# Optimization experiments

Hardware: AMD Instinct MI355X
Metric: run time of the kernel (lower is better)

## Reference

```python
import jax, jax.numpy as jnp
import numpy as np

WIDTH = 1024
NH = 16
HD = 64
MBS = 16
B = 4
L = 2048
BASE_LR = 1.0
EPS = 1e-6


def gelu_tanh(x):
    return jax.nn.gelu(x, approximate=True)


def gelu_bwd(x):
    t = jnp.tanh(0.79788456 * x * (1 + 0.044715 * x * x))
    return 0.5 * x * ((1 - t * t) * (0.79788456 + 0.1070322243 * x * x)) + 0.5 * (1 + t)


def ln_fwd(x, g, b):
    mu = x.mean(-1, keepdims=True)
    var = ((x - mu) ** 2).mean(-1, keepdims=True)
    return g * ((x - mu) * jax.lax.rsqrt(var + EPS)) + b


def ln_l2_bwd(x, tgt, g, b):
    # grad of 0.5*||LN(x)-tgt||^2 wrt x
    mu = x.mean(-1, keepdims=True)
    var = ((x - mu) ** 2).mean(-1, keepdims=True)
    std = jnp.sqrt(var + EPS)
    xh = (x - mu) / std
    gx = (g * xh + b - tgt) * g
    return (gx - gx.mean(-1, keepdims=True) - xh * (gx * xh).mean(-1, keepdims=True)) / std


def adapter_forward(hidden_states, Wq, Wk, Wv, Wo, Wg, lr_w, lr_b,
                    learnable_token_idx, norm_w, norm_b, W1, b1, W2, b2,
                    post_w, post_b):
    Bb, Ll, width = hidden_states.shape
    nh, hd = norm_w.shape
    mbs = learnable_token_idx.shape[0]
    nc = Ll // mbs  # L chosen divisible by mini_batch_size

    def split_heads(x):  # [B,L,width] -> [B,nh,nc,mbs,hd]
        return x.reshape(Bb, Ll, nh, hd).transpose(0, 2, 1, 3).reshape(Bb, nh, nc, mbs, hd)

    XQ = split_heads(hidden_states @ Wq.T)
    XK = split_heads(hidden_states @ Wk.T)
    XV = split_heads(hidden_states @ Wv.T)

    # eta: learnable per-token lr gate (get_eta)
    X = hidden_states.reshape(Bb, nc, mbs, width)
    lr = jnp.einsum('bnkc,hdc->bhnkd', X, lr_w) + lr_b.reshape(1, nh, 1, 1, 1)
    lr = jax.nn.sigmoid(lr).transpose(0, 1, 2, 4, 3)  # [B,nh,nc,1,mbs]
    lr_eta = BASE_LR * lr / hd
    token_idx = jnp.clip(1.0 / jnp.arange(1, mbs + 1, dtype=hidden_states.dtype)
                         + learnable_token_idx, 0.0, None)
    token_eta = token_idx.reshape(1, 1, 1, mbs, 1)
    eta = token_eta * lr_eta  # [B,nh,nc,mbs,mbs]

    tril = jnp.tril(jnp.ones((mbs, mbs), dtype=hidden_states.dtype))
    lnw = norm_w.reshape(nh, 1, hd)
    lnb = norm_b.reshape(nh, 1, hd)

    def step(carry, xs):
        W1s, b1s, W2s, b2s = carry  # [B,nh,hd,4hd], [B,nh,1,4hd], [B,nh,4hd,hd], [B,nh,1,hd]
        XQm, XKm, XVm, etam = xs    # [B,nh,mbs,hd] x3, [B,nh,mbs,mbs]
        X1 = XKm
        Z1 = X1 @ W1s + b1s
        X2 = gelu_tanh(Z1)
        Z2 = X2 @ W2s + b2s
        gZ2 = ln_l2_bwd(Z2, XVm - XKm, lnw, lnb)
        gZ1 = (gZ2 @ jnp.swapaxes(W2s, -1, -2)) * gelu_bwd(Z1)
        eta_tril = etam * tril
        Attn1 = tril * (XQm @ jnp.swapaxes(X1, -1, -2))
        b1_bar = b1s - eta_tril @ gZ1
        Z1_bar = XQm @ W1s - (etam * Attn1) @ gZ1 + b1_bar
        X2_bar = gelu_tanh(Z1_bar)
        Attn2 = tril * (X2_bar @ jnp.swapaxes(X2, -1, -2))
        b2_bar = b2s - eta_tril @ gZ2
        Z2_bar = X2_bar @ W2s - (etam * Attn2) @ gZ2 + b2_bar
        last = etam[:, :, -1, :, None]  # [B,nh,mbs,1]
        W1n = W1s - jnp.swapaxes(last * X1, -1, -2) @ gZ1
        b1n = b1s - (last * gZ1).sum(-2, keepdims=True)
        W2n = W2s - jnp.swapaxes(last * X2, -1, -2) @ gZ2
        b2n = b2s - (last * gZ2).sum(-2, keepdims=True)
        XQW = XQm + ln_fwd(Z2_bar, lnw, lnb)
        return (W1n, b1n, W2n, b2n), XQW

    carry0 = (jnp.broadcast_to(W1, (Bb,) + W1.shape),
              jnp.broadcast_to(b1, (Bb,) + b1.shape),
              jnp.broadcast_to(W2, (Bb,) + W2.shape),
              jnp.broadcast_to(b2, (Bb,) + b2.shape))
    xs = tuple(jnp.moveaxis(t, 2, 0) for t in (XQ, XK, XV, eta))
    _, XQW = jax.lax.scan(step, carry0, xs)  # [nc,B,nh,mbs,hd]
    out = XQW.transpose(1, 0, 3, 2, 4).reshape(Bb, Ll, width)

    # post_norm (LayerNorm eps=1e-6)
    out = ln_fwd(out, post_w, post_b)
    # gate
    out = gelu_tanh(hidden_states @ Wg.T) * out
    # o_proj
    return out @ Wo.T


def setup_inputs():
    key = jax.random.key(0)
    ks = jax.random.split(key, 10)
    n = lambda k, s: jax.random.normal(k, s, dtype=jnp.float32) * 0.02
    return {
        'hidden_states': jax.random.normal(ks[0], (B, L, WIDTH), dtype=jnp.float32),
        'Wq': n(ks[1], (WIDTH, WIDTH)),
        'Wk': n(ks[2], (WIDTH, WIDTH)),
        'Wv': n(ks[3], (WIDTH, WIDTH)),
        'Wo': n(ks[4], (WIDTH, WIDTH)),
        'Wg': n(ks[5], (WIDTH, WIDTH)),
        'lr_w': n(ks[6], (NH, 1, WIDTH)),
        'lr_b': jnp.zeros((NH, 1), jnp.float32),
        'learnable_token_idx': jnp.zeros((MBS,), jnp.float32),
        'norm_w': jnp.ones((NH, HD), jnp.float32),
        'norm_b': jnp.zeros((NH, HD), jnp.float32),
        'W1': n(ks[7], (NH, HD, 4 * HD)),
        'b1': jnp.zeros((NH, 1, 4 * HD), jnp.float32),
        'W2': n(ks[8], (NH, 4 * HD, HD)),
        'b2': jnp.zeros((NH, 1, HD), jnp.float32),
        'post_w': jnp.ones((WIDTH,), jnp.float32),
        'post_b': jnp.zeros((WIDTH,), jnp.float32),
    }


def reference(hidden_states, Wq, Wk, Wv, Wo, Wg, lr_w, lr_b, learnable_token_idx,
              norm_w, norm_b, W1, b1, W2, b2, post_w, post_b):
    return adapter_forward(hidden_states, Wq, Wk, Wv, Wo, Wg, lr_w, lr_b,
                           learnable_token_idx, norm_w, norm_b, W1, b1, W2, b2,
                           post_w, post_b)
```

## Files before the change

kernel.cpp:

```cpp
#include <hip/hip_runtime.h>

#define WIDTH 1024
#define MBSZ 16
#define LLL 2048
#define NCHUNK 128

typedef __attribute__((ext_vector_type(4))) float f32x4;
typedef __attribute__((ext_vector_type(2))) float f32x2;
typedef __attribute__((ext_vector_type(8))) short short8;
typedef __attribute__((ext_vector_type(4))) short short4v;
typedef __attribute__((ext_vector_type(2))) unsigned u32x2;
typedef __attribute__((ext_vector_type(4))) unsigned u32x4;

#define MFMA16(a, b, c) __builtin_amdgcn_mfma_f32_16x16x32_bf16((a), (b), (c), 0, 0, 0)

__device__ __forceinline__ short f2bf(float f) {
  unsigned u = __float_as_uint(f);
  u = (u + 0x7FFFu + ((u >> 16) & 1u)) >> 16;
  return (short)u;
}
__device__ __forceinline__ float bf2f(short s) {
  return __uint_as_float(((unsigned)(unsigned short)s) << 16);
}
__device__ __forceinline__ unsigned cvt_pk(float lo, float hi) {
  unsigned r;
  asm("v_cvt_pk_bf16_f32 %0, %1, %2" : "=v"(r) : "v"(lo), "v"(hi));
  return r;
}
__device__ __forceinline__ float fast_e2u(float x) {
  return __builtin_amdgcn_exp2f(x * (2.30220776f + 0.10294322f * x * x));
}
__device__ __forceinline__ float gelu_f(float x) {
  float e = fast_e2u(x);
  return x * (1.0f - __builtin_amdgcn_rcpf(e + 1.0f));
}
__device__ __forceinline__ float gelu_bwd_f(float x) {
  float e = fast_e2u(x);
  float r = __builtin_amdgcn_rcpf(e + 1.0f);
  return 2.0f * x * r * (1.0f - r) * (0.79788456f + 0.1070322243f * x * x) + (1.0f - r);
}
__device__ __forceinline__ int w2row(int d) { return d * 264 + (d >> 3) * 24; }

__global__ __launch_bounds__(256) void cvt_kernel(const float* __restrict__ hs,
                                                  const float* __restrict__ Wq,
                                                  const float* __restrict__ Wk,
                                                  const float* __restrict__ Wv,
                                                  const float* __restrict__ Wg,
                                                  const float* __restrict__ Wo,
                                                  short* __restrict__ dst) {
  const long idx = ((long)blockIdx.x * 256 + threadIdx.x) * 8;
  if (idx >= 13631488L) return;
  const float* src;
  long off;
  if (idx < 8388608L)       { src = hs; off = idx; }
  else if (idx < 9437184L)  { src = Wq; off = idx - 8388608L; }
  else if (idx < 10485760L) { src = Wk; off = idx - 9437184L; }
  else if (idx < 11534336L) { src = Wv; off = idx - 10485760L; }
  else if (idx < 12582912L) { src = Wg; off = idx - 11534336L; }
  else                      { src = Wo; off = idx - 12582912L; }
  const f32x4 a = *(const f32x4*)(src + off);
  const f32x4 b = *(const f32x4*)(src + off + 4);
  u32x4 o;
  o[0] = cvt_pk(a[0], a[1]); o[1] = cvt_pk(a[2], a[3]);
  o[2] = cvt_pk(b[0], b[1]); o[3] = cvt_pk(b[2], b[3]);
  *(u32x4*)(dst + idx) = o;
}

template <int OUTBF>
__global__ __launch_bounds__(256) void gemm_bt_b(const short* __restrict__ A,
                                                 const short* __restrict__ W,
                                                 float* __restrict__ C,
                                                 short* __restrict__ Cb) {
  __shared__ __align__(16) short sA[64][40];
  __shared__ __align__(16) short sB[64][40];
  const int tid = threadIdx.x;
  const int m0 = blockIdx.x * 64, n0 = blockIdx.y * 64;
  const int srow = tid >> 2, sk = (tid & 3) * 8;
  const int wv = tid >> 6, ln = tid & 63;
  const int fr = ln & 15, kh = (ln >> 4) * 8;
  f32x4 acc[4];
#pragma unroll
  for (int s = 0; s < 4; ++s) acc[s] = (f32x4){0.f, 0.f, 0.f, 0.f};
  const short* ga = A + (long)(m0 + srow) * 1024 + sk;
  const short* gw = W + (long)(n0 + srow) * 1024 + sk;
  for (int k0 = 0; k0 < 1024; k0 += 32) {
    const short8 a8 = *(const short8*)(ga + k0);
    const short8 w8 = *(const short8*)(gw + k0);
    *(short8*)&sA[srow][sk] = a8;
    *(short8*)&sB[srow][sk] = w8;
    __syncthreads();
    short8 af = *(const short8*)&sA[wv * 16 + fr][kh];
#pragma unroll
    for (int s = 0; s < 4; ++s) {
      short8 bf8 = *(const short8*)&sB[s * 16 + fr][kh];
      acc[s] = MFMA16(af, bf8, acc[s]);
    }
    __syncthreads();
  }
  const int orow = m0 + wv * 16 + (ln >> 4) * 4;
#pragma unroll
  for (int s = 0; s < 4; ++s)
#pragma unroll
    for (int q = 0; q < 4; ++q) {
      if (OUTBF)
        Cb[(long)(orow + q) * 1024 + n0 + s * 16 + fr] = f2bf(acc[s][q]);
      else
        C[(long)(orow + q) * 1024 + n0 + s * 16 + fr] = acc[s][q];
    }
}

__global__ __launch_bounds__(256) void lr_kernel(const float* __restrict__ hs,
                                                 const float* __restrict__ lrw,
                                                 const float* __restrict__ lrb,
                                                 float* __restrict__ out) {
  __shared__ __align__(16) float row[1024];
  const int t = blockIdx.x, tid = threadIdx.x;
  *(f32x4*)&row[tid * 4] = *(const f32x4*)&hs[(long)t * 1024 + tid * 4];
  __syncthreads();
  const int hh = tid >> 4, j = tid & 15;
  const float* wrow = lrw + hh * 1024;
  float s = 0.f;
#pragma unroll 4
  for (int m = 0; m < 16; ++m) {
    const int c = j * 4 + m * 64;
    f32x4 x = *(const f32x4*)&row[c];
    f32x4 w = *(const f32x4*)&wrow[c];
    s += x[0] * w[0] + x[1] * w[1] + x[2] * w[2] + x[3] * w[3];
  }
#pragma unroll
  for (int o = 8; o; o >>= 1) s += __shfl_xor(s, o, 16);
  if (j == 0) {
    const float v = s + lrb[hh];
    const float sg = 1.f / (1.f + expf(-v));
    const int b = t >> 11, tr = t & 2047;
    out[((b << 4) + hh) * 2048 + tr] = sg * (1.f / 64.f);
  }
}

__global__ __launch_bounds__(512, 2) void scan_kernel(
    float* __restrict__ Qb, const float* __restrict__ Kb, const float* __restrict__ Vb,
    const float* __restrict__ LRb, const float* __restrict__ lti,
    const float* __restrict__ nw, const float* __restrict__ nb,
    const float* __restrict__ W1in, const float* __restrict__ b1in,
    const float* __restrict__ W2in, const float* __restrict__ b2in) {
  __shared__ __align__(16) short sW1b[256 * 72];
  __shared__ __align__(16) short sW2dp[64 * 264 + 192];
  __shared__ __align__(16) short la1T[64 * 24];
  __shared__ __align__(16) short la2T[256 * 24];
  __shared__ __align__(16) short sX1b[16 * 72];
  __shared__ __align__(16) short sXQb[16 * 72];
  __shared__ __align__(16) float sXQf[16 * 68];
  __shared__ __align__(16) float sTg[16 * 72];
  __shared__ __align__(16) short sX2b[16 * 264];
  __shared__ __align__(16) short sXbb[16 * 264];
  __shared__ __align__(16) short sG1c[256 * 24];
  __shared__ __align__(16) short sG2b[16 * 72];
  __shared__ __align__(16) short sG2c[64 * 24];
  __shared__ __align__(16) float sZ2f[16 * 68];
  __shared__ __align__(16) short sC1b[16 * 24];
  __shared__ __align__(16) short sC2b[16 * 24];
  __shared__ __align__(16) float sB1[256];
  __shared__ __align__(16) float sB2[64];
  __shared__ float sLr[16];
  __shared__ float sTok[16];
  __shared__ __align__(16) float sLnw[64];
  __shared__ __align__(16) float sLnb[64];

  const int bh = blockIdx.x, b = bh >> 4, h = bh & 15;
  const int tid = threadIdx.x;
  const int w = tid >> 6, ln = tid & 63;
  const int fr = ln & 15, half = ln >> 4, hk = half * 8;
  const int nt0 = 2 * w;

  float w1m[8][4], w2m[8][4];
#pragma unroll
  for (int r = 0; r < 8; ++r) {
    const int T = w * 8 + r, dt = T >> 4, pt = T & 15;
#pragma unroll
    for (int qq = 0; qq < 4; ++qq) {
      w1m[r][qq] = W1in[h * 16384 + (dt * 16 + half * 4 + qq) * 256 + pt * 16 + fr];
      w2m[r][qq] = W2in[h * 16384 + (pt * 16 + half * 4 + qq) * 64 + dt * 16 + fr];
    }
  }
  for (int e = tid; e < 16384; e += 512) {
    {
      const int d = e >> 8, p = e & 255;
      sW1b[p * 72 + d] = f2bf(W1in[h * 16384 + e]);
    }
    {
      const int p = e >> 6, d = e & 63;
      sW2dp[w2row(d) + (p ^ (((d >> 3) & 3) << 3))] = f2bf(W2in[h * 16384 + e]);
    }
  }
  if (tid < 256) sB1[tid] = b1in[h * 256 + tid];
  if (tid < 64) { sB2[tid] = b2in[h * 64 + tid]; sLnw[tid] = nw[h * 64 + tid]; sLnb[tid] = nb[h * 64 + tid]; }
  if (tid < 16) sTok[tid] = fmaxf(1.0f / (float)(tid + 1) + lti[tid], 0.0f);

  const f32x4 zf4 = (f32x4){0.f, 0.f, 0.f, 0.f};
  short8 zs8;
#pragma unroll
  for (int j = 0; j < 8; ++j) zs8[j] = 0;

  const int pf_i = tid >> 5;
  const int pf_d = (tid & 31) * 2;
  f32x2 pk, pq, pv;
  float plr = 0.f;
  {
    const long a0 = ((long)(b * LLL + pf_i)) * WIDTH + h * 64 + pf_d;
    pk = *(const f32x2*)&Kb[a0];
    pq = *(const f32x2*)&Qb[a0];
    pv = *(const f32x2*)&Vb[a0];
    if (tid < 16) plr = LRb[(long)bh * 2048 + tid];
  }

  for (int n = 0; n < NCHUNK; ++n) {
    const long gbase = ((long)(b * LLL + n * MBSZ)) * WIDTH + h * 64;

    {
      *(unsigned*)&sX1b[pf_i * 72 + pf_d] = cvt_pk(pk[0], pk[1]);
      *(unsigned*)&sXQb[pf_i * 72 + pf_d] = cvt_pk(pq[0], pq[1]);
      sXQf[pf_i * 68 + pf_d] = pq[0];
      sXQf[pf_i * 68 + pf_d + 1] = pq[1];
      sTg[pf_i * 72 + pf_d] = pv[0] - pk[0];
      sTg[pf_i * 72 + pf_d + 1] = pv[1] - pk[1];
      if (tid < 16) sLr[tid] = plr;
    }
    __syncthreads();

    short8 aX1[2], aXQ[2];
    aX1[0] = *(const short8*)&sX1b[fr * 72 + hk];
    aX1[1] = *(const short8*)&sX1b[fr * 72 + 32 + hk];
    aXQ[0] = *(const short8*)&sXQb[fr * 72 + hk];
    aXQ[1] = *(const short8*)&sXQb[fr * 72 + 32 + hk];
    f32x4 z1[2], q1[2];
    float b1p[2];
#pragma unroll
    for (int t = 0; t < 2; ++t) {
      const int p = (nt0 + t) * 16 + fr;
      z1[t] = zf4; q1[t] = zf4;
#pragma unroll
      for (int ks = 0; ks < 2; ++ks) {
        short8 bw = *(const short8*)&sW1b[p * 72 + ks * 32 + hk];
        z1[t] = MFMA16(aX1[ks], bw, z1[t]);
        q1[t] = MFMA16(aXQ[ks], bw, q1[t]);
      }
      b1p[t] = sB1[p];
#pragma unroll
      for (int qq = 0; qq < 4; ++qq) {
        z1[t][qq] += b1p[t];
        sX2b[(half * 4 + qq) * 264 + p] = f2bf(gelu_f(z1[t][qq]));
      }
    }
    {
      const float tok15 = sTok[15];
      const int d = tid >> 3, j0 = (tid & 7) * 2;
      const float v0 = bf2f(sX1b[j0 * 72 + d]) * (tok15 * sLr[j0]);
      const float v1 = bf2f(sX1b[(j0 + 1) * 72 + d]) * (tok15 * sLr[j0 + 1]);
      *(unsigned*)&la1T[d * 24 + j0] = cvt_pk(v0, v1);
    }
    if (w == 0) {
      f32x4 c = MFMA16(aXQ[0], aX1[0], zf4);
      c = MFMA16(aXQ[1], aX1[1], c);
#pragma unroll
      for (int qq = 0; qq < 4; ++qq) {
        const int i = half * 4 + qq, j = fr;
        sC1b[i * 24 + j] = f2bf((i >= j) ? sTok[i] * sLr[j] * (c[qq] + 1.0f) : 0.0f);
      }
    }
    __syncthreads();

    float bb2old = 0.f;
    if (w < 4) {
      const int d = w * 16 + fr;
      const int sw = ((d >> 3) & 3) << 3;
      const int rb = w2row(d);
      f32x4 za = zf4, zb = zf4;
#pragma unroll
      for (int ks = 0; ks < 4; ++ks) {
        short8 a = *(const short8*)&sX2b[fr * 264 + ks * 32 + hk];
        short8 bfr = *(const short8*)&sW2dp[rb + ((ks * 32 + hk) ^ sw)];
        za = MFMA16(a, bfr, za);
      }
#pragma unroll
      for (int ks = 4; ks < 8; ++ks) {
        short8 a = *(const short8*)&sX2b[fr * 264 + ks * 32 + hk];
        short8 bfr = *(const short8*)&sW2dp[rb + ((ks * 32 + hk) ^ sw)];
        zb = MFMA16(a, bfr, zb);
      }
      bb2old = sB2[d];
#pragma unroll
      for (int qq = 0; qq < 4; ++qq)
        sZ2f[(half * 4 + qq) * 68 + d] = za[qq] + zb[qq] + bb2old;
    }
    __syncthreads();

    if (tid < 256) {
      const int i = tid >> 4, j4 = tid & 15;
      const f32x4 z = *(const f32x4*)&sZ2f[i * 68 + j4 * 4];
      float s1 = z[0] + z[1] + z[2] + z[3];
      float s2 = z[0] * z[0] + z[1] * z[1] + z[2] * z[2] + z[3] * z[3];
#pragma unroll
      for (int o = 8; o; o >>= 1) { s1 += __shfl_xor(s1, o, 16); s2 += __shfl_xor(s2, o, 16); }
      const float mu = s1 * (1.f / 64.f);
      const float rstd = rsqrtf(s2 * (1.f / 64.f) - mu * mu + 1e-6f);
      const f32x4 g = *(const f32x4*)&sLnw[j4 * 4];
      const f32x4 bb = *(const f32x4*)&sLnb[j4 * 4];
      const f32x4 tg = *(const f32x4*)&sTg[i * 72 + j4 * 4];
      f32x4 xh, gx;
      float a1 = 0.f, a2 = 0.f;
#pragma unroll
      for (int e = 0; e < 4; ++e) {
        xh[e] = (z[e] - mu) * rstd;
        gx[e] = (g[e] * xh[e] + bb[e] - tg[e]) * g[e];
        a1 += gx[e]; a2 += gx[e] * xh[e];
      }
#pragma unroll
      for (int o = 8; o; o >>= 1) { a1 += __shfl_xor(a1, o, 16); a2 += __shfl_xor(a2, o, 16); }
      const float m1 = a1 * (1.f / 64.f), m2 = a2 * (1.f / 64.f);
      float o4[4];
#pragma unroll
      for (int e = 0; e < 4; ++e) o4[e] = (gx[e] - m1 - xh[e] * m2) * rstd;
      const unsigned lo = cvt_pk(o4[0], o4[1]);
      const unsigned hi = cvt_pk(o4[2], o4[3]);
      *(u32x2*)&sG2b[i * 72 + j4 * 4] = (u32x2){lo, hi};
      sG2c[(j4 * 4 + 0) * 24 + i] = (short)lo;
      sG2c[(j4 * 4 + 1) * 24 + i] = (short)(lo >> 16);
      sG2c[(j4 * 4 + 2) * 24 + i] = (short)hi;
      sG2c[(j4 * 4 + 3) * 24 + i] = (short)(hi >> 16);
    } else {
      const int pp = tid - 256;
      const float tok15 = sTok[15];
      unsigned uu[8];
#pragma unroll
      for (int jp = 0; jp < 8; ++jp) {
        const float v0 = bf2f(sX2b[(2 * jp) * 264 + pp]) * (tok15 * sLr[2 * jp]);
        const float v1 = bf2f(sX2b[(2 * jp + 1) * 264 + pp]) * (tok15 * sLr[2 * jp + 1]);
        uu[jp] = cvt_pk(v0, v1);
      }
      *(u32x4*)&la2T[pp * 24] = (u32x4){uu[0], uu[1], uu[2], uu[3]};
      *(u32x4*)&la2T[pp * 24 + 8] = (u32x4){uu[4], uu[5], uu[6], uu[7]};
    }
    __syncthreads();

    {
      short8 aG2[2];
      aG2[0] = *(const short8*)&sG2b[fr * 72 + hk];
      aG2[1] = *(const short8*)&sG2b[fr * 72 + 32 + hk];
#pragma unroll
      for (int t = 0; t < 2; ++t) {
        const int p = (nt0 + t) * 16 + fr;
        f32x4 g = zf4;
#pragma unroll
        for (int ks = 0; ks < 2; ++ks) {
          const int dg = ks * 32 + hk;
          const int rb = w2row(dg) + (p ^ (((dg >> 3) & 3) << 3));
          short8 bw;
#pragma unroll
          for (int jj = 0; jj < 8; ++jj) bw[jj] = sW2dp[rb + jj * 264];
          g = MFMA16(aG2[ks], bw, g);
        }
        const unsigned lo = cvt_pk(g[0] * gelu_bwd_f(z1[t][0]), g[1] * gelu_bwd_f(z1[t][1]));
        const unsigned hi = cvt_pk(g[2] * gelu_bwd_f(z1[t][2]), g[3] * gelu_bwd_f(z1[t][3]));
        *(u32x2*)&sG1c[p * 24 + half * 4] = (u32x2){lo, hi};
      }
    }
    if (tid < 64) {
      float s = 0.f;
#pragma unroll
      for (int j = 0; j < 16; ++j) s += sLr[j] * bf2f(sG2c[tid * 24 + j]);
      sB2[tid] -= sTok[15] * s;
    }
    __syncthreads();

    {
      short8 ac = zs8;
      if (half < 2) ac = *(const short8*)&sC1b[fr * 24 + hk];
#pragma unroll
      for (int t = 0; t < 2; ++t) {
        const int p = (nt0 + t) * 16 + fr;
        short8 bg = zs8;
        if (half < 2) bg = *(const short8*)&sG1c[p * 24 + hk];
        f32x4 corr = MFMA16(ac, bg, zf4);
#pragma unroll
        for (int qq = 0; qq < 4; ++qq)
          sXbb[(half * 4 + qq) * 264 + p] = f2bf(gelu_f(q1[t][qq] + b1p[t] - corr[qq]));
      }
    }
    {
#pragma unroll
      for (int r = 0; r < 8; ++r) {
        const int T = w * 8 + r, dt = T >> 4, pt = T & 15;
        short8 af = zs8, bg = zs8;
        if (half < 2) {
          af = *(const short8*)&la1T[(dt * 16 + fr) * 24 + hk];
          bg = *(const short8*)&sG1c[(pt * 16 + fr) * 24 + hk];
        }
        f32x4 dl = MFMA16(af, bg, zf4);
        const int pp = pt * 16 + fr, d0 = dt * 16 + half * 4;
        w1m[r][0] -= dl[0]; w1m[r][1] -= dl[1]; w1m[r][2] -= dl[2]; w1m[r][3] -= dl[3];
        const unsigned lo = cvt_pk(w1m[r][0], w1m[r][1]);
        const unsigned hi = cvt_pk(w1m[r][2], w1m[r][3]);
        *(u32x2*)&sW1b[pp * 72 + d0] = (u32x2){lo, hi};
      }
    }
    if (tid < 256) {
      float s = 0.f;
#pragma unroll
      for (int j = 0; j < 16; ++j) s += sLr[j] * bf2f(sG1c[tid * 24 + j]);
      sB1[tid] -= sTok[15] * s;
    }
    __syncthreads();

    {
      const int nn = (n + 1 < NCHUNK) ? n + 1 : n;
      const long a1 = ((long)(b * LLL + nn * MBSZ + pf_i)) * WIDTH + h * 64 + pf_d;
      pk = *(const f32x2*)&Kb[a1];
      pq = *(const f32x2*)&Qb[a1];
      pv = *(const f32x2*)&Vb[a1];
      if (tid < 16) plr = LRb[(long)bh * 2048 + nn * MBSZ + tid];
    }
    f32x4 zbar = zf4;
    if (w < 4) {
      const int d = w * 16 + fr;
      const int sw = ((d >> 3) & 3) << 3;
      const int rb = w2row(d);
      f32x4 za = zf4, zb = zf4;
#pragma unroll
      for (int ks = 0; ks < 4; ++ks) {
        short8 a = *(const short8*)&sXbb[fr * 264 + ks * 32 + hk];
        short8 bfr = *(const short8*)&sW2dp[rb + ((ks * 32 + hk) ^ sw)];
        za = MFMA16(a, bfr, za);
      }
#pragma unroll
      for (int ks = 4; ks < 8; ++ks) {
        short8 a = *(const short8*)&sXbb[fr * 264 + ks * 32 + hk];
        short8 bfr = *(const short8*)&sW2dp[rb + ((ks * 32 + hk) ^ sw)];
        zb = MFMA16(a, bfr, zb);
      }
      zbar[0] = za[0] + zb[0]; zbar[1] = za[1] + zb[1];
      zbar[2] = za[2] + zb[2]; zbar[3] = za[3] + zb[3];
    } else if (w == 4) {
      f32x4 c = zf4;
#pragma unroll
      for (int ks = 0; ks < 8; ++ks) {
        short8 a = *(const short8*)&sXbb[fr * 264 + ks * 32 + hk];
        short8 bx = *(const short8*)&sX2b[fr * 264 + ks * 32 + hk];
        c = MFMA16(a, bx, c);
      }
#pragma unroll
      for (int qq = 0; qq < 4; ++qq) {
        const int i = half * 4 + qq, j = fr;
        sC2b[i * 24 + j] = f2bf((i >= j) ? sTok[i] * sLr[j] * (c[qq] + 1.0f) : 0.0f);
      }
    }
    __syncthreads();

    if (w < 4) {
      const int d = w * 16 + fr;
      short8 ac = zs8, bg = zs8;
      if (half < 2) {
        ac = *(const short8*)&sC2b[fr * 24 + hk];
        bg = *(const short8*)&sG2c[d * 24 + hk];
      }
      f32x4 corr = MFMA16(ac, bg, zf4);
#pragma unroll
      for (int qq = 0; qq < 4; ++qq)
        sZ2f[(half * 4 + qq) * 68 + d] = zbar[qq] + bb2old - corr[qq];
    }
    {
#pragma unroll
      for (int r = 0; r < 8; ++r) {
        const int T = w * 8 + r, pt = T & 15, dt = T >> 4;
        short8 af = zs8, bg = zs8;
        if (half < 2) {
          af = *(const short8*)&la2T[(pt * 16 + fr) * 24 + hk];
          bg = *(const short8*)&sG2c[(dt * 16 + fr) * 24 + hk];
        }
        f32x4 dl = MFMA16(af, bg, zf4);
        const int dd = dt * 16 + fr;
        const int swp = ((dd >> 3) & 3) << 3;
        const int p0 = pt * 16 + half * 4;
        w2m[r][0] -= dl[0]; w2m[r][1] -= dl[1]; w2m[r][2] -= dl[2]; w2m[r][3] -= dl[3];
        const unsigned lo = cvt_pk(w2m[r][0], w2m[r][1]);
        const unsigned hi = cvt_pk(w2m[r][2], w2m[r][3]);
        *(u32x2*)&sW2dp[w2row(dd) + (p0 ^ swp)] = (u32x2){lo, hi};
      }
    }
    __syncthreads();

    if (tid < 256) {
      const int i = tid >> 4, j4 = tid & 15;
      const f32x4 z = *(const f32x4*)&sZ2f[i * 68 + j4 * 4];
      float s1 = z[0] + z[1] + z[2] + z[3];
      float s2 = z[0] * z[0] + z[1] * z[1] + z[2] * z[2] + z[3] * z[3];
#pragma unroll
      for (int o = 8; o; o >>= 1) { s1 += __shfl_xor(s1, o, 16); s2 += __shfl_xor(s2, o, 16); }
      const float mu = s1 * (1.f / 64.f);
      const float rstd = rsqrtf(s2 * (1.f / 64.f) - mu * mu + 1e-6f);
      const f32x4 g = *(const f32x4*)&sLnw[j4 * 4];
      const f32x4 bb = *(const f32x4*)&sLnb[j4 * 4];
      const f32x4 xq = *(const f32x4*)&sXQf[i * 68 + j4 * 4];
      f32x4 o4;
#pragma unroll
      for (int e = 0; e < 4; ++e) o4[e] = xq[e] + g[e] * ((z[e] - mu) * rstd) + bb[e];
      *(f32x4*)&Qb[gbase + (long)i * WIDTH + j4 * 4] = o4;
    }
    __syncthreads();
  }
}

__global__ __launch_bounds__(256) void epi_kernel(const float* __restrict__ X,
                                                  const short* __restrict__ G,
                                                  const float* __restrict__ pw,
                                                  const float* __restrict__ pb,
                                                  short* __restrict__ T) {
  __shared__ float red[8];
  const int t = blockIdx.x, tid = threadIdx.x;
  const long base = (long)t * 1024 + tid * 4;
  f32x4 x = *(const f32x4*)&X[base];
  float s1 = x[0] + x[1] + x[2] + x[3];
  float s2 = x[0] * x[0] + x[1] * x[1] + x[2] * x[2] + x[3] * x[3];
#pragma unroll
  for (int o = 32; o; o >>= 1) { s1 += __shfl_xor(s1, o, 64); s2 += __shfl_xor(s2, o, 64); }
  const int wv = tid >> 6, ln = tid & 63;
  if (ln == 0) { red[wv] = s1; red[4 + wv] = s2; }
  __syncthreads();
  s1 = red[0] + red[1] + red[2] + red[3];
  s2 = red[4] + red[5] + red[6] + red[7];
  const float mu = s1 * (1.f / 1024.f);
  const float rstd = rsqrtf(s2 * (1.f / 1024.f) - mu * mu + 1e-6f);
  const short4v g4 = *(const short4v*)&G[base];
  f32x4 w = *(const f32x4*)&pw[tid * 4];
  f32x4 bb = *(const f32x4*)&pb[tid * 4];
  float o4[4];
#pragma unroll
  for (int e = 0; e < 4; ++e) {
    float y = w[e] * ((x[e] - mu) * rstd) + bb[e];
    o4[e] = gelu_f(bf2f(g4[e])) * y;
  }
  *(u32x2*)&T[base] = (u32x2){cvt_pk(o4[0], o4[1]), cvt_pk(o4[2], o4[3])};
}

extern "C" void kernel_launch(void* const* d_in, const int* in_sizes, int n_in,
                              void* d_out, int out_size, void* d_ws, size_t ws_size,
                              hipStream_t stream) {
  const float* hs  = (const float*)d_in[0];
  const float* Wq  = (const float*)d_in[1];
  const float* Wk  = (const float*)d_in[2];
  const float* Wv  = (const float*)d_in[3];
  const float* Wo  = (const float*)d_in[4];
  const float* Wg  = (const float*)d_in[5];
  const float* lrw = (const float*)d_in[6];
  const float* lrb = (const float*)d_in[7];
  const float* lti = (const float*)d_in[8];
  const float* nw  = (const float*)d_in[9];
  const float* nb  = (const float*)d_in[10];
  const float* W1  = (const float*)d_in[11];
  const float* b1  = (const float*)d_in[12];
  const float* W2  = (const float*)d_in[13];
  const float* b2  = (const float*)d_in[14];
  const float* pw  = (const float*)d_in[15];
  const float* pb  = (const float*)d_in[16];
  float* out = (float*)d_out;
  float* ws = (float*)d_ws;

  float* Qb  = ws;
  float* Kb  = ws + 8388608;
  float* Vb  = ws + 16777216;
  float* LRb = ws + 25165824;
  short* hsb = (short*)(ws + 25296896);
  short* Wqb = hsb + 8388608;
  short* Wkb = Wqb + 1048576;
  short* Wvb = Wkb + 1048576;
  short* Wgb = Wvb + 1048576;
  short* Wob = Wgb + 1048576;
  short* Tb  = (short*)Kb;
  short* Gbb = (short*)Vb;

  dim3 gg(128, 16);
  cvt_kernel<<<6656, 256, 0, stream>>>(hs, Wq, Wk, Wv, Wg, Wo, hsb);
  gemm_bt_b<0><<<gg, 256, 0, stream>>>(hsb, Wqb, Qb, nullptr);
  gemm_bt_b<0><<<gg, 256, 0, stream>>>(hsb, Wkb, Kb, nullptr);
  gemm_bt_b<0><<<gg, 256, 0, stream>>>(hsb, Wvb, Vb, nullptr);
  lr_kernel<<<8192, 256, 0, stream>>>(hs, lrw, lrb, LRb);
  scan_kernel<<<64, 512, 0, stream>>>(Qb, Kb, Vb, LRb, lti, nw, nb, W1, b1, W2, b2);
  gemm_bt_b<1><<<gg, 256, 0, stream>>>(hsb, Wgb, nullptr, Gbb);
  epi_kernel<<<8192, 256, 0, stream>>>(Qb, Gbb, pw, pb, Tb);
  gemm_bt_b<0><<<gg, 256, 0, stream>>>(Tb, Wob, out, nullptr);
}
```

Measured before the change: 990.9 us.

## Fuse QKV and lr gemms, overlap gate gemm with scan, widen gemm tiles

Q, K, V projections and the lr gate are merged into one launch, and gemm tiles grow from 64x64 to 64x128. The gate gemm now runs as extra blocks inside the scan launch, so it uses CUs left idle by the 64 scan blocks. Inside the scan, the W2 forward is split across all 8 waves with partial sums, the layernorm backward uses all 512 threads, la2T construction moves to idle threads in a later phase, and bias-gradient reductions use vector loads. The goal is fewer launches and less serial latency in the scan, at the cost of more shared-memory traffic and extra syncs.

```diff
diff --git a/kernel.cpp b/kernel.cpp
--- a/kernel.cpp
+++ b/kernel.cpp
@@ -40,6 +40,49 @@
   return 2.0f * x * r * (1.0f - r) * (0.79788456f + 0.1070322243f * x * x) + (1.0f - r);
 }
 __device__ __forceinline__ int w2row(int d) { return d * 264 + (d >> 3) * 24; }
+
+template <int OUTBF>
+__device__ __forceinline__ void gemm_64x128(const short* __restrict__ A,
+                                            const short* __restrict__ W,
+                                            float* __restrict__ C,
+                                            short* __restrict__ Cb,
+                                            int m0, int n0,
+                                            short* sA, short* sB, int t2) {
+  const int wv = t2 >> 6, ln = t2 & 63;
+  const int fr = ln & 15, kh = (ln >> 4) * 8;
+  const int arow = t2 >> 2, aseg = (t2 & 3) * 8;
+  f32x4 acc[8];
+#pragma unroll
+  for (int s = 0; s < 8; ++s) acc[s] = (f32x4){0.f, 0.f, 0.f, 0.f};
+  const short* ga = A + (long)(m0 + arow) * 1024 + aseg;
+  const short* gw0 = W + (long)(n0 + arow) * 1024 + aseg;
+  const short* gw1 = W + (long)(n0 + 64 + arow) * 1024 + aseg;
+  for (int k0 = 0; k0 < 1024; k0 += 32) {
+    const short8 a8 = *(const short8*)(ga + k0);
+    const short8 w80 = *(const short8*)(gw0 + k0);
+    const short8 w81 = *(const short8*)(gw1 + k0);
+    *(short8*)&sA[arow * 40 + aseg] = a8;
+    *(short8*)&sB[arow * 40 + aseg] = w80;
+    *(short8*)&sB[(arow + 64) * 40 + aseg] = w81;
+    __syncthreads();
+    const short8 af = *(const short8*)&sA[(wv * 16 + fr) * 40 + kh];
+#pragma unroll
+    for (int s = 0; s < 8; ++s) {
+      const short8 bf8 = *(const short8*)&sB[(s * 16 + fr) * 40 + kh];
+      acc[s] = MFMA16(af, bf8, acc[s]);
+    }
+    __syncthreads();
+  }
+  const int orow = m0 + wv * 16 + (ln >> 4) * 4;
+#pragma unroll
+  for (int s = 0; s < 8; ++s)
+#pragma unroll
+    for (int q = 0; q < 4; ++q) {
+      const long off = (long)(orow + q) * 1024 + n0 + s * 16 + fr;
+      if (OUTBF) Cb[off] = f2bf(acc[s][q]);
+      else C[off] = acc[s][q];
+    }
+}
 
 __global__ __launch_bounds__(256) void cvt_kernel(const float* __restrict__ hs,
                                                   const float* __restrict__ Wq,
@@ -66,83 +109,68 @@
   *(u32x4*)(dst + idx) = o;
 }
 
-template <int OUTBF>
-__global__ __launch_bounds__(256) void gemm_bt_b(const short* __restrict__ A,
-                                                 const short* __restrict__ W,
-                                                 float* __restrict__ C,
-                                                 short* __restrict__ Cb) {
-  __shared__ __align__(16) short sA[64][40];
-  __shared__ __align__(16) short sB[64][40];
+__global__ __launch_bounds__(256) void gemm_final(const short* __restrict__ A,
+                                                  const short* __restrict__ W,
+                                                  float* __restrict__ C) {
+  __shared__ __align__(16) short sA[2560];
+  __shared__ __align__(16) short sB[5120];
+  gemm_64x128<0>(A, W, C, nullptr, blockIdx.x * 64, blockIdx.y * 128, sA, sB, threadIdx.x);
+}
+
+__global__ __launch_bounds__(256) void qkv_lr_kernel(const short* __restrict__ hsb,
+                                                     const short* __restrict__ Wqb,
+                                                     const short* __restrict__ Wkb,
+                                                     const short* __restrict__ Wvb,
+                                                     float* __restrict__ Qb,
+                                                     float* __restrict__ Kb,
+                                                     float* __restrict__ Vb,
+                                                     const float* __restrict__ hs,
+                                                     const float* __restrict__ lrw,
+                                                     const float* __restrict__ lrb,
+                                                     float* __restrict__ LRb) {
+  __shared__ __align__(16) short sA[2560];
+  __shared__ __align__(16) short sB[5120];
+  __shared__ __align__(16) float row[1024];
   const int tid = threadIdx.x;
-  const int m0 = blockIdx.x * 64, n0 = blockIdx.y * 64;
-  const int srow = tid >> 2, sk = (tid & 3) * 8;
-  const int wv = tid >> 6, ln = tid & 63;
-  const int fr = ln & 15, kh = (ln >> 4) * 8;
-  f32x4 acc[4];
-#pragma unroll
-  for (int s = 0; s < 4; ++s) acc[s] = (f32x4){0.f, 0.f, 0.f, 0.f};
-  const short* ga = A + (long)(m0 + srow) * 1024 + sk;
-  const short* gw = W + (long)(n0 + srow) * 1024 + sk;
-  for (int k0 = 0; k0 < 1024; k0 += 32) {
-    const short8 a8 = *(const short8*)(ga + k0);
-    const short8 w8 = *(const short8*)(gw + k0);
-    *(short8*)&sA[srow][sk] = a8;
-    *(short8*)&sB[srow][sk] = w8;
-    __syncthreads();
-    short8 af = *(const short8*)&sA[wv * 16 + fr][kh];
-#pragma unroll
-    for (int s = 0; s < 4; ++s) {
-      short8 bf8 = *(const short8*)&sB[s * 16 + fr][kh];
-      acc[s] = MFMA16(af, bf8, acc[s]);
-    }
-    __syncthreads();
-  }
-  const int orow = m0 + wv * 16 + (ln >> 4) * 4;
-#pragma unroll
-  for (int s = 0; s < 4; ++s)
-#pragma unroll
-    for (int q = 0; q < 4; ++q) {
-      if (OUTBF)
-        Cb[(long)(orow + q) * 1024 + n0 + s * 16 + fr] = f2bf(acc[s][q]);
-      else
-        C[(long)(orow + q) * 1024 + n0 + s * 16 + fr] = acc[s][q];
-    }
-}
-
-__global__ __launch_bounds__(256) void lr_kernel(const float* __restrict__ hs,
-                                                 const float* __restrict__ lrw,
-                                                 const float* __restrict__ lrb,
-                                                 float* __restrict__ out) {
-  __shared__ __align__(16) float row[1024];
-  const int t = blockIdx.x, tid = threadIdx.x;
-  *(f32x4*)&row[tid * 4] = *(const f32x4*)&hs[(long)t * 1024 + tid * 4];
-  __syncthreads();
-  const int hh = tid >> 4, j = tid & 15;
-  const float* wrow = lrw + hh * 1024;
-  float s = 0.f;
+  const int idx = blockIdx.x;
+  if (idx < 3072) {
+    const int which = idx >> 10, t = idx & 1023;
+    const short* W = (which == 0) ? Wqb : (which == 1) ? Wkb : Wvb;
+    float* C = (which == 0) ? Qb : (which == 1) ? Kb : Vb;
+    gemm_64x128<0>(hsb, W, C, nullptr, (t & 127) * 64, (t >> 7) * 128, sA, sB, tid);
+  } else {
+    const int t = idx - 3072;
+    *(f32x4*)&row[tid * 4] = *(const f32x4*)&hs[(long)t * 1024 + tid * 4];
+    __syncthreads();
+    const int hh = tid >> 4, j = tid & 15;
+    const float* wrow = lrw + hh * 1024;
+    float s = 0.f;
 #pragma unroll 4
-  for (int m = 0; m < 16; ++m) {
-    const int c = j * 4 + m * 64;
-    f32x4 x = *(const f32x4*)&row[c];
-    f32x4 w = *(const f32x4*)&wrow[c];
-    s += x[0] * w[0] + x[1] * w[1] + x[2] * w[2] + x[3] * w[3];
-  }
-#pragma unroll
-  for (int o = 8; o; o >>= 1) s += __shfl_xor(s, o, 16);
-  if (j == 0) {
-    const float v = s + lrb[hh];
-    const float sg = 1.f / (1.f + expf(-v));
-    const int b = t >> 11, tr = t & 2047;
-    out[((b << 4) + hh) * 2048 + tr] = sg * (1.f / 64.f);
-  }
-}
-
-__global__ __launch_bounds__(512, 2) void scan_kernel(
+    for (int m = 0; m < 16; ++m) {
+      const int c = j * 4 + m * 64;
+      f32x4 x = *(const f32x4*)&row[c];
+      f32x4 w = *(const f32x4*)&wrow[c];
+      s += x[0] * w[0] + x[1] * w[1] + x[2] * w[2] + x[3] * w[3];
+    }
+#pragma unroll
+    for (int o = 8; o; o >>= 1) s += __shfl_xor(s, o, 16);
+    if (j == 0) {
+      const float v = s + lrb[hh];
+      const float sg = 1.f / (1.f + expf(-v));
+      const int b = t >> 11, tr = t & 2047;
+      LRb[((b << 4) + hh) * 2048 + tr] = sg * (1.f / 64.f);
+    }
+  }
+}
+
+__global__ __launch_bounds__(512, 2) void scan_gate_kernel(
     float* __restrict__ Qb, const float* __restrict__ Kb, const float* __restrict__ Vb,
     const float* __restrict__ LRb, const float* __restrict__ lti,
     const float* __restrict__ nw, const float* __restrict__ nb,
     const float* __restrict__ W1in, const float* __restrict__ b1in,
-    const float* __restrict__ W2in, const float* __restrict__ b2in) {
+    const float* __restrict__ W2in, const float* __restrict__ b2in,
+    const short* __restrict__ hsA, const short* __restrict__ Wgb,
+    short* __restrict__ Gout) {
   __shared__ __align__(16) short sW1b[256 * 72];
   __shared__ __align__(16) short sW2dp[64 * 264 + 192];
   __shared__ __align__(16) short la1T[64 * 24];
@@ -156,6 +184,8 @@
   __shared__ __align__(16) short sG1c[256 * 24];
   __shared__ __align__(16) short sG2b[16 * 72];
   __shared__ __align__(16) short sG2c[64 * 24];
+  __shared__ __align__(16) float sZ2p0[16 * 68];
+  __shared__ __align__(16) float sZ2p1[16 * 68];
   __shared__ __align__(16) float sZ2f[16 * 68];
   __shared__ __align__(16) short sC1b[16 * 24];
   __shared__ __align__(16) short sC2b[16 * 24];
@@ -166,8 +196,18 @@
   __shared__ __align__(16) float sLnw[64];
   __shared__ __align__(16) float sLnb[64];
 
+  const int tid = threadIdx.x;
+
+  if (blockIdx.x >= 64) {
+    const int hh = tid >> 8, t2 = tid & 255;
+    const int tile = (blockIdx.x - 64) * 2 + hh;
+    short* sAh = sW1b + hh * 7680;
+    short* sBh = sAh + 2560;
+    gemm_64x128<1>(hsA, Wgb, nullptr, Gout, (tile & 127) * 64, (tile >> 7) * 128, sAh, sBh, t2);
+    return;
+  }
+
   const int bh = blockIdx.x, b = bh >> 4, h = bh & 15;
-  const int tid = threadIdx.x;
   const int w = tid >> 6, ln = tid & 63;
   const int fr = ln & 15, half = ln >> 4, hk = half * 8;
   const int nt0 = 2 * w;
@@ -270,75 +310,67 @@
     __syncthreads();
 
     float bb2old = 0.f;
-    if (w < 4) {
-      const int d = w * 16 + fr;
+    {
+      const int dt = w & 3, k2 = w >> 2;
+      const int d = dt * 16 + fr;
       const int sw = ((d >> 3) & 3) << 3;
       const int rb = w2row(d);
       f32x4 za = zf4, zb = zf4;
 #pragma unroll
-      for (int ks = 0; ks < 4; ++ks) {
+      for (int ks = k2 * 4; ks < k2 * 4 + 2; ++ks) {
         short8 a = *(const short8*)&sX2b[fr * 264 + ks * 32 + hk];
         short8 bfr = *(const short8*)&sW2dp[rb + ((ks * 32 + hk) ^ sw)];
         za = MFMA16(a, bfr, za);
       }
 #pragma unroll
-      for (int ks = 4; ks < 8; ++ks) {
+      for (int ks = k2 * 4 + 2; ks < k2 * 4 + 4; ++ks) {
         short8 a = *(const short8*)&sX2b[fr * 264 + ks * 32 + hk];
         short8 bfr = *(const short8*)&sW2dp[rb + ((ks * 32 + hk) ^ sw)];
         zb = MFMA16(a, bfr, zb);
       }
-      bb2old = sB2[d];
+      float* dst = k2 ? sZ2p1 : sZ2p0;
 #pragma unroll
       for (int qq = 0; qq < 4; ++qq)
-        sZ2f[(half * 4 + qq) * 68 + d] = za[qq] + zb[qq] + bb2old;
-    }
-    __syncthreads();
-
-    if (tid < 256) {
-      const int i = tid >> 4, j4 = tid & 15;
-      const f32x4 z = *(const f32x4*)&sZ2f[i * 68 + j4 * 4];
-      float s1 = z[0] + z[1] + z[2] + z[3];
-      float s2 = z[0] * z[0] + z[1] * z[1] + z[2] * z[2] + z[3] * z[3];
-#pragma unroll
-      for (int o = 8; o; o >>= 1) { s1 += __shfl_xor(s1, o, 16); s2 += __shfl_xor(s2, o, 16); }
+        dst[(half * 4 + qq) * 68 + d] = za[qq] + zb[qq];
+      if (w < 4) bb2old = sB2[w * 16 + fr];
+    }
+    __syncthreads();
+
+    {
+      const int i = tid >> 5, j2 = tid & 31;
+      const int e0 = j2 * 2;
+      const f32x2 zp0 = *(const f32x2*)&sZ2p0[i * 68 + e0];
+      const f32x2 zp1 = *(const f32x2*)&sZ2p1[i * 68 + e0];
+      const f32x2 b2v = *(const f32x2*)&sB2[e0];
+      f32x2 z;
+      z[0] = zp0[0] + zp1[0] + b2v[0];
+      z[1] = zp0[1] + zp1[1] + b2v[1];
+      float s1 = z[0] + z[1];
+      float s2 = z[0] * z[0] + z[1] * z[1];
+#pragma unroll
+      for (int o = 16; o; o >>= 1) { s1 += __shfl_xor(s1, o, 32); s2 += __shfl_xor(s2, o, 32); }
       const float mu = s1 * (1.f / 64.f);
       const float rstd = rsqrtf(s2 * (1.f / 64.f) - mu * mu + 1e-6f);
-      const f32x4 g = *(const f32x4*)&sLnw[j4 * 4];
-      const f32x4 bb = *(const f32x4*)&sLnb[j4 * 4];
-      const f32x4 tg = *(const f32x4*)&sTg[i * 72 + j4 * 4];
-      f32x4 xh, gx;
+      const f32x2 g = *(const f32x2*)&sLnw[e0];
+      const f32x2 bb = *(const f32x2*)&sLnb[e0];
+      const f32x2 tg = *(const f32x2*)&sTg[i * 72 + e0];
+      f32x2 xh, gx;
       float a1 = 0.f, a2 = 0.f;
 #pragma unroll
-      for (int e = 0; e < 4; ++e) {
+      for (int e = 0; e < 2; ++e) {
         xh[e] = (z[e] - mu) * rstd;
         gx[e] = (g[e] * xh[e] + bb[e] - tg[e]) * g[e];
         a1 += gx[e]; a2 += gx[e] * xh[e];
       }
 #pragma unroll
-      for (int o = 8; o; o >>= 1) { a1 += __shfl_xor(a1, o, 16); a2 += __shfl_xor(a2, o, 16); }
+      for (int o = 16; o; o >>= 1) { a1 += __shfl_xor(a1, o, 32); a2 += __shfl_xor(a2, o, 32); }
       const float m1 = a1 * (1.f / 64.f), m2 = a2 * (1.f / 64.f);
-      float o4[4];
-#pragma unroll
-      for (int e = 0; e < 4; ++e) o4[e] = (gx[e] - m1 - xh[e] * m2) * rstd;
-      const unsigned lo = cvt_pk(o4[0], o4[1]);
-      const unsigned hi = cvt_pk(o4[2], o4[3]);
-      *(u32x2*)&sG2b[i * 72 + j4 * 4] = (u32x2){lo, hi};
-      sG2c[(j4 * 4 + 0) * 24 + i] = (short)lo;
-      sG2c[(j4 * 4 + 1) * 24 + i] = (short)(lo >> 16);
-      sG2c[(j4 * 4 + 2) * 24 + i] = (short)hi;
-      sG2c[(j4 * 4 + 3) * 24 + i] = (short)(hi >> 16);
-    } else {
-      const int pp = tid - 256;
-      const float tok15 = sTok[15];
-      unsigned uu[8];
-#pragma unroll
-      for (int jp = 0; jp < 8; ++jp) {
-        const float v0 = bf2f(sX2b[(2 * jp) * 264 + pp]) * (tok15 * sLr[2 * jp]);
-        const float v1 = bf2f(sX2b[(2 * jp + 1) * 264 + pp]) * (tok15 * sLr[2 * jp + 1]);
-        uu[jp] = cvt_pk(v0, v1);
-      }
-      *(u32x4*)&la2T[pp * 24] = (u32x4){uu[0], uu[1], uu[2], uu[3]};
-      *(u32x4*)&la2T[pp * 24 + 8] = (u32x4){uu[4], uu[5], uu[6], uu[7]};
+      const float o0 = (gx[0] - m1 - xh[0] * m2) * rstd;
+      const float o1 = (gx[1] - m1 - xh[1] * m2) * rstd;
+      const unsigned lo = cvt_pk(o0, o1);
+      *(unsigned*)&sG2b[i * 72 + e0] = lo;
+      sG2c[(e0 + 0) * 24 + i] = (short)lo;
+      sG2c[(e0 + 1) * 24 + i] = (short)(lo >> 16);
     }
     __syncthreads();
 
@@ -353,10 +385,10 @@
 #pragma unroll
         for (int ks = 0; ks < 2; ++ks) {
           const int dg = ks * 32 + hk;
-          const int rb = w2row(dg) + (p ^ (((dg >> 3) & 3) << 3));
+          const int rb2 = w2row(dg) + (p ^ (((dg >> 3) & 3) << 3));
           short8 bw;
 #pragma unroll
-          for (int jj = 0; jj < 8; ++jj) bw[jj] = sW2dp[rb + jj * 264];
+          for (int jj = 0; jj < 8; ++jj) bw[jj] = sW2dp[rb2 + jj * 264];
           g = MFMA16(aG2[ks], bw, g);
         }
         const unsigned lo = cvt_pk(g[0] * gelu_bwd_f(z1[t][0]), g[1] * gelu_bwd_f(z1[t][1]));
@@ -367,7 +399,12 @@
     if (tid < 64) {
       float s = 0.f;
 #pragma unroll
-      for (int j = 0; j < 16; ++j) s += sLr[j] * bf2f(sG2c[tid * 24 + j]);
+      for (int k = 0; k < 4; ++k) {
+        const short4v g4 = *(const short4v*)&sG2c[tid * 24 + k * 4];
+        const f32x4 lr4 = *(const f32x4*)&sLr[k * 4];
+        s += lr4[0] * bf2f(g4[0]) + lr4[1] * bf2f(g4[1]) +
+             lr4[2] * bf2f(g4[2]) + lr4[3] * bf2f(g4[3]);
+      }
       sB2[tid] -= sTok[15] * s;
     }
     __syncthreads();
@@ -406,7 +443,12 @@
     if (tid < 256) {
       float s = 0.f;
 #pragma unroll
-      for (int j = 0; j < 16; ++j) s += sLr[j] * bf2f(sG1c[tid * 24 + j]);
+      for (int k = 0; k < 4; ++k) {
+        const short4v g4 = *(const short4v*)&sG1c[tid * 24 + k * 4];
+        const f32x4 lr4 = *(const f32x4*)&sLr[k * 4];
+        s += lr4[0] * bf2f(g4[0]) + lr4[1] * bf2f(g4[1]) +
+             lr4[2] * bf2f(g4[2]) + lr4[3] * bf2f(g4[3]);
+      }
       sB1[tid] -= sTok[15] * s;
     }
     __syncthreads();
@@ -451,6 +493,19 @@
       for (int qq = 0; qq < 4; ++qq) {
         const int i = half * 4 + qq, j = fr;
         sC2b[i * 24 + j] = f2bf((i >= j) ? sTok[i] * sLr[j] * (c[qq] + 1.0f) : 0.0f);
+      }
+    } else {
+      const float tok15 = sTok[15];
+      for (int pp = tid - 320; pp < 256; pp += 192) {
+        unsigned uu[8];
+#pragma unroll
+        for (int jp = 0; jp < 8; ++jp) {
+          const float v0 = bf2f(sX2b[(2 * jp) * 264 + pp]) * (tok15 * sLr[2 * jp]);
+          const float v1 = bf2f(sX2b[(2 * jp + 1) * 264 + pp]) * (tok15 * sLr[2 * jp + 1]);
+          uu[jp] = cvt_pk(v0, v1);
+        }
+        *(u32x4*)&la2T[pp * 24] = (u32x4){uu[0], uu[1], uu[2], uu[3]};
+        *(u32x4*)&la2T[pp * 24 + 8] = (u32x4){uu[4], uu[5], uu[6], uu[7]};
       }
     }
     __syncthreads();
@@ -488,22 +543,23 @@
     }
     __syncthreads();
 
-    if (tid < 256) {
-      const int i = tid >> 4, j4 = tid & 15;
-      const f32x4 z = *(const f32x4*)&sZ2f[i * 68 + j4 * 4];
-      float s1 = z[0] + z[1] + z[2] + z[3];
-      float s2 = z[0] * z[0] + z[1] * z[1] + z[2] * z[2] + z[3] * z[3];
-#pragma unroll
-      for (int o = 8; o; o >>= 1) { s1 += __shfl_xor(s1, o, 16); s2 += __shfl_xor(s2, o, 16); }
+    {
+      const int i = tid >> 5, j2 = tid & 31;
+      const int e0 = j2 * 2;
+      const f32x2 z = *(const f32x2*)&sZ2f[i * 68 + e0];
+      float s1 = z[0] + z[1];
+      float s2 = z[0] * z[0] + z[1] * z[1];
+#pragma unroll
+      for (int o = 16; o; o >>= 1) { s1 += __shfl_xor(s1, o, 32); s2 += __shfl_xor(s2, o, 32); }
       const float mu = s1 * (1.f / 64.f);
       const float rstd = rsqrtf(s2 * (1.f / 64.f) - mu * mu + 1e-6f);
-      const f32x4 g = *(const f32x4*)&sLnw[j4 * 4];
-      const f32x4 bb = *(const f32x4*)&sLnb[j4 * 4];
-      const f32x4 xq = *(const f32x4*)&sXQf[i * 68 + j4 * 4];
-      f32x4 o4;
-#pragma unroll
-      for (int e = 0; e < 4; ++e) o4[e] = xq[e] + g[e] * ((z[e] - mu) * rstd) + bb[e];
-      *(f32x4*)&Qb[gbase + (long)i * WIDTH + j4 * 4] = o4;
+      const f32x2 g = *(const f32x2*)&sLnw[e0];
+      const f32x2 bb = *(const f32x2*)&sLnb[e0];
+      const f32x2 xq = *(const f32x2*)&sXQf[i * 68 + e0];
+      f32x2 o2;
+      o2[0] = xq[0] + g[0] * ((z[0] - mu) * rstd) + bb[0];
+      o2[1] = xq[1] + g[1] * ((z[1] - mu) * rstd) + bb[1];
+      *(f32x2*)&Qb[gbase + (long)i * WIDTH + e0] = o2;
     }
     __syncthreads();
   }
@@ -575,16 +631,12 @@
   short* Wgb = Wvb + 1048576;
   short* Wob = Wgb + 1048576;
   short* Tb  = (short*)Kb;
-  short* Gbb = (short*)Vb;
-
-  dim3 gg(128, 16);
+  short* Gbb = (short*)out;
+
   cvt_kernel<<<6656, 256, 0, stream>>>(hs, Wq, Wk, Wv, Wg, Wo, hsb);
-  gemm_bt_b<0><<<gg, 256, 0, stream>>>(hsb, Wqb, Qb, nullptr);
-  gemm_bt_b<0><<<gg, 256, 0, stream>>>(hsb, Wkb, Kb, nullptr);
-  gemm_bt_b<0><<<gg, 256, 0, stream>>>(hsb, Wvb, Vb, nullptr);
-  lr_kernel<<<8192, 256, 0, stream>>>(hs, lrw, lrb, LRb);
-  scan_kernel<<<64, 512, 0, stream>>>(Qb, Kb, Vb, LRb, lti, nw, nb, W1, b1, W2, b2);
-  gemm_bt_b<1><<<gg, 256, 0, stream>>>(hsb, Wgb, nullptr, Gbb);
+  qkv_lr_kernel<<<11264, 256, 0, stream>>>(hsb, Wqb, Wkb, Wvb, Qb, Kb, Vb, hs, lrw, lrb, LRb);
+  scan_gate_kernel<<<576, 512, 0, stream>>>(Qb, Kb, Vb, LRb, lti, nw, nb, W1, b1, W2, b2,
+                                            hsb, Wgb, Gbb);
   epi_kernel<<<8192, 256, 0, stream>>>(Qb, Gbb, pw, pb, Tb);
-  gemm_bt_b<0><<<gg, 256, 0, stream>>>(Tb, Wob, out, nullptr);
-}
+  gemm_final<<<dim3(128, 8), 256, 0, stream>>>(Tb, Wob, out);
+}
```

After: 953.4 us. 3.8% less time.
